# Performance work log

Hardware: AMD Instinct MI355X
Metric: run time of the kernel (lower is better)

## Reference

```python
import jax, jax.numpy as jnp
import numpy as np

MAX_LENGTH = 128
SOS_TOKEN = 0

V, H, B, S = 16384, 512, 32, 128


def gru_cell(x, h, Wih, Whh, bih, bhh):
    # torch nn.GRU gate layout: [r, z, n]
    gi = x @ Wih.T + bih  # [B, 3H]
    gh = h @ Whh.T + bhh  # [B, 3H]
    ir, iz, inn = jnp.split(gi, 3, axis=-1)
    hr, hz, hn = jnp.split(gh, 3, axis=-1)
    r = jax.nn.sigmoid(ir + hr)
    z = jax.nn.sigmoid(iz + hz)
    n = jnp.tanh(inn + r * hn)
    return (1.0 - z) * n + z * h


def setup_inputs() -> dict:
    key = jax.random.key(0)
    ks = jax.random.split(key, 13)
    w = lambda k, shape: (jax.random.normal(k, shape, dtype=jnp.float32) * 0.1)
    return {
        "input_tensor": jax.random.randint(ks[0], (B, S), 0, V),
        "enc_emb": w(ks[1], (V, H)),
        "enc_Wih": w(ks[2], (3 * H, H)),
        "enc_Whh": w(ks[3], (3 * H, H)),
        "enc_bih": w(ks[4], (3 * H,)),
        "enc_bhh": w(ks[5], (3 * H,)),
        "dec_emb": w(ks[6], (V, H)),
        "dec_Wih": w(ks[7], (3 * H, H)),
        "dec_Whh": w(ks[8], (3 * H, H)),
        "dec_bih": w(ks[9], (3 * H,)),
        "dec_bhh": w(ks[10], (3 * H,)),
        "out_W": w(ks[11], (V, H)),
        "out_b": w(ks[12], (V,)),
    }


def reference(input_tensor, enc_emb, enc_Wih, enc_Whh, enc_bih, enc_bhh,
              dec_emb, dec_Wih, dec_Whh, dec_bih, dec_bhh, out_W, out_b):
    batch = input_tensor.shape[0]

    # ---- encoder: embedding + GRU over source sequence ----
    xs = enc_emb[input_tensor]                 # [B, S, H]
    xs = jnp.swapaxes(xs, 0, 1)                # [S, B, H]

    def enc_step(h, x):
        h = gru_cell(x, h, enc_Wih, enc_Whh, enc_bih, enc_bhh)
        return h, h

    h0 = jnp.zeros((batch, H), dtype=xs.dtype)
    enc_hidden, enc_outputs = jax.lax.scan(enc_step, h0, xs)
    # enc_outputs: [S, B, H] (unused downstream, as in the original)

    # ---- decoder: free-run (target_tensor=None) with argmax feedback ----
    sos = jnp.full((batch,), SOS_TOKEN, dtype=jnp.int32)

    def dec_step(carry, _):
        h, tok = carry
        x = dec_emb[tok]                       # [B, H]
        h = gru_cell(x, h, dec_Wih, dec_Whh, dec_bih, dec_bhh)
        logits = h @ out_W.T + out_b           # [B, V]
        tok = jnp.argmax(logits, axis=-1).astype(jnp.int32)  # topk(1) feedback
        return (h, tok), logits

    (dec_hidden, _), logits = jax.lax.scan(dec_step, (enc_hidden, sos), None,
                                           length=MAX_LENGTH)
    logits = jnp.swapaxes(logits, 0, 1)        # [B, MAX_LENGTH, V]
    log_probs = jax.nn.log_softmax(logits, axis=-1)
    return log_probs, dec_hidden
```

## Files before the change

kernel.cpp:

```cpp
#include <hip/hip_runtime.h>

#define HDIM 512
#define BATCH 32
#define SEQ 128
#define VOCAB 16384
#define NBLK 256
#define NGRU 128
#define NTHR 256
#define SLOTP 32
#define HLDS_W 516

typedef unsigned long long u64;
typedef unsigned int u32;

static __device__ __forceinline__ u64 aload64(const u64* p) {
    return __hip_atomic_load(p, __ATOMIC_RELAXED, __HIP_MEMORY_SCOPE_AGENT);
}
static __device__ __forceinline__ void astore64(u64* p, u64 v) {
    __hip_atomic_store(p, v, __ATOMIC_RELAXED, __HIP_MEMORY_SCOPE_AGENT);
}
static __device__ __forceinline__ u32 aload32(const u32* p) {
    return __hip_atomic_load(p, __ATOMIC_RELAXED, __HIP_MEMORY_SCOPE_AGENT);
}
static __device__ __forceinline__ void astore32(u32* p, u32 v) {
    __hip_atomic_store(p, v, __ATOMIC_RELAXED, __HIP_MEMORY_SCOPE_AGENT);
}
static __device__ __forceinline__ void astore32f(float* p, float v) {
    __hip_atomic_store((u32*)p, __float_as_uint(v), __ATOMIC_RELAXED,
                       __HIP_MEMORY_SCOPE_AGENT);
}

static __device__ __forceinline__ float4 ld4(const float* p) {
    return *reinterpret_cast<const float4*>(p);
}
static __device__ __forceinline__ float dot4(float4 a, float4 b) {
    return a.x*b.x + a.y*b.y + a.z*b.z + a.w*b.w;
}
static __device__ __forceinline__ u32 ford(float f) {
    u32 b = __float_as_uint(f);
    return b ^ ((b >> 31) ? 0xFFFFFFFFu : 0x80000000u);
}
static __device__ __forceinline__ u64 shfl_xor_u64(u64 x, int m) {
    int lo = __shfl_xor((int)(u32)x, m);
    int hi = __shfl_xor((int)(u32)(x >> 32), m);
    return ((u64)(u32)hi << 32) | (u32)lo;
}

static __device__ __forceinline__ void pollN(const u32* slots, u32 target,
                                             int tid, int nslots) {
    if (tid < 64) {
        const int per = (nslots + 63) >> 6;
        int it = 0;
        for (;;) {
            bool ok = true;
            for (int k = 0; k < per; ++k) {
                int idx = tid * per + k;
                if (idx < nslots)
                    ok &= (aload32(&slots[idx * SLOTP]) >= target);
            }
            if (__ballot(ok) == ~0ull) break;
            if (it > 64)      __builtin_amdgcn_s_sleep(16);
            else if (it > 8)  __builtin_amdgcn_s_sleep(2);
            ++it;
        }
    }
    __syncthreads();
    asm volatile("" ::: "memory");
}

static __device__ __forceinline__ void stage_wide(float* hlf, const float* hsrc,
                                                  int tid, int blk) {
    const int rot = (blk & 63) * 64;
    #pragma unroll
    for (int g = 0; g < 2; ++g) {
        float4 v[8];
        int qs[8];
        #pragma unroll
        for (int k = 0; k < 8; ++k) {
            int q = ((g * 8 + k) * NTHR + tid + rot) & 4095;
            qs[k] = q;
            asm volatile("global_load_dwordx4 %0, %1, off sc1"
                         : "=v"(v[k]) : "v"(hsrc + q * 4));
        }
        asm volatile("s_waitcnt vmcnt(0)" ::: "memory");
        __builtin_amdgcn_sched_barrier(0);
        #pragma unroll
        for (int k = 0; k < 8; ++k) {
            int w = qs[k] * 4;
            *reinterpret_cast<float4*>(hlf + (w >> 9) * HLDS_W + (w & 511)) = v[k];
        }
    }
}

static __device__ __forceinline__ void stage_h(float* hlf, const float* hglob, int tid) {
    const u64* src = (const u64*)hglob;
    #pragma unroll
    for (int it = 0; it < 32; ++it) {
        int q = it * 256 + tid;
        int w = q * 2;
        u64 v = aload64(src + q);
        *reinterpret_cast<u64*>(hlf + (w >> 9) * HLDS_W + (w & 511)) = v;
    }
}

static __device__ __forceinline__ void gru_j(
    int j, int tid, const int* toks, const float* hlf, float* hout,
    const float* __restrict__ Wih, const float* __restrict__ Whh,
    const float* __restrict__ bih, const float* __restrict__ bhh,
    const float* __restrict__ emb)
{
    const int lane = tid & 63;
    const int kh   = lane >> 5;
    const int b    = lane & 31;

    const int tok = toks[b];
    const float* xrow = emb + (size_t)tok * HDIM + kh * 256;
    const float* hrow = hlf + b * HLDS_W + kh * 256;
    const float* wir = Wih + (size_t)(0*HDIM + j) * HDIM + kh * 256;
    const float* wiz = Wih + (size_t)(1*HDIM + j) * HDIM + kh * 256;
    const float* win = Wih + (size_t)(2*HDIM + j) * HDIM + kh * 256;
    const float* whr = Whh + (size_t)(0*HDIM + j) * HDIM + kh * 256;
    const float* whz = Whh + (size_t)(1*HDIM + j) * HDIM + kh * 256;
    const float* whn = Whh + (size_t)(2*HDIM + j) * HDIM + kh * 256;

    float pr = 0.f, pz = 0.f, pxn = 0.f, phn = 0.f;
    #pragma unroll 4
    for (int k4 = 0; k4 < 64; ++k4) {
        float4 x4 = ld4(xrow + k4*4);
        float4 h4 = ld4(hrow + k4*4);
        pr  += dot4(x4, ld4(wir + k4*4)) + dot4(h4, ld4(whr + k4*4));
        pz  += dot4(x4, ld4(wiz + k4*4)) + dot4(h4, ld4(whz + k4*4));
        pxn += dot4(x4, ld4(win + k4*4));
        phn += dot4(h4, ld4(whn + k4*4));
    }
    pr  += __shfl_xor(pr, 32);
    pz  += __shfl_xor(pz, 32);
    pxn += __shfl_xor(pxn, 32);
    phn += __shfl_xor(phn, 32);

    if (kh == 0) {
        float r = 1.f / (1.f + expf(-(pr + bih[j]      + bhh[j])));
        float z = 1.f / (1.f + expf(-(pz + bih[HDIM+j] + bhh[HDIM+j])));
        float n = tanhf(pxn + bih[2*HDIM+j] + r * (phn + bhh[2*HDIM+j]));
        float hprev = hlf[b * HLDS_W + j];
        astore32f(hout + b * HDIM + j, (1.f - z) * n + z * hprev);
    }
}

static __device__ __forceinline__ void argmax_finalize(
    int tid, const u64* pk, u64 (*redk)[8], int* tok_s)
{
    const int fb = tid >> 3, kc = tid & 7;
    const u64* p = pk + fb * NBLK;
    u64 best = aload64(p + kc);
    #pragma unroll 4
    for (int k = 1; k < 32; ++k) {
        u64 x = aload64(p + kc + k * 8);
        if (x > best) best = x;
    }
    redk[fb][kc] = best;
    __syncthreads();
    if (tid < BATCH) {
        u64 bb = redk[tid][0];
        #pragma unroll
        for (int c = 1; c < 8; ++c) { u64 x = redk[tid][c]; if (x > bb) bb = x; }
        tok_s[tid] = (int)(~(u32)bb);
    }
}

static __device__ __forceinline__ void softmax_row(float* p, int tid,
                                                   float* redm, float* reds) {
    float4 vals[16];
    float m = -3.4e38f;
    #pragma unroll
    for (int i = 0; i < 16; ++i) {
        vals[i] = ld4(p + (i * 256 + tid) * 4);
        m = fmaxf(m, fmaxf(fmaxf(vals[i].x, vals[i].y), fmaxf(vals[i].z, vals[i].w)));
    }
    #pragma unroll
    for (int d = 1; d < 64; d <<= 1) m = fmaxf(m, __shfl_xor(m, d));
    if ((tid & 63) == 0) redm[tid >> 6] = m;
    __syncthreads();
    m = fmaxf(fmaxf(redm[0], redm[1]), fmaxf(redm[2], redm[3]));
    float s = 0.f;
    #pragma unroll
    for (int i = 0; i < 16; ++i) {
        s += expf(vals[i].x - m) + expf(vals[i].y - m)
           + expf(vals[i].z - m) + expf(vals[i].w - m);
    }
    #pragma unroll
    for (int d = 1; d < 64; d <<= 1) s += __shfl_xor(s, d);
    if ((tid & 63) == 0) reds[tid >> 6] = s;
    __syncthreads();
    s = reds[0] + reds[1] + reds[2] + reds[3];
    const float lg = m + logf(s);
    #pragma unroll
    for (int i = 0; i < 16; ++i) {
        float4 r;
        r.x = vals[i].x - lg; r.y = vals[i].y - lg;
        r.z = vals[i].z - lg; r.w = vals[i].w - lg;
        *reinterpret_cast<float4*>(p + (i * 256 + tid) * 4) = r;
    }
    __syncthreads();
}

__global__ __launch_bounds__(NTHR, 1) void seq2seq_main(
    const int* __restrict__ input,
    const float* __restrict__ enc_emb, const float* __restrict__ enc_Wih,
    const float* __restrict__ enc_Whh, const float* __restrict__ enc_bih,
    const float* __restrict__ enc_bhh,
    const float* __restrict__ dec_emb, const float* __restrict__ dec_Wih,
    const float* __restrict__ dec_Whh, const float* __restrict__ dec_bih,
    const float* __restrict__ dec_bhh,
    const float* __restrict__ out_W, const float* __restrict__ out_b,
    float* __restrict__ out, float* hglob, u64* pk,
    u32* hslot, u32* pkslot)
{
    __shared__ __align__(16) float hl[BATCH][HLDS_W];
    __shared__ __align__(16) float part[4][64][33];
    __shared__ int tok_s[BATCH];
    __shared__ u64 redk[BATCH][8];

    const int tid = threadIdx.x;
    const int blk = blockIdx.x;
    float* hlf = &hl[0][0];

    for (int i = tid; i < BATCH * HLDS_W; i += NTHR) hlf[i] = 0.f;
    __syncthreads();

    const int w = tid >> 6;
    const int l = tid & 63;

    if (blk < NGRU) {
        for (int t = 0; t < SEQ; ++t) {
            float* hgo = hglob + ((t + 1) & 1) * (BATCH * HDIM);
            if (tid < BATCH) tok_s[tid] = input[tid * SEQ + t];
            __syncthreads();
            gru_j(blk * 4 + w, tid, tok_s, hlf, hgo,
                  enc_Wih, enc_Whh, enc_bih, enc_bhh, enc_emb);
            __syncthreads();
            if (tid == 0) astore32(&hslot[blk * SLOTP], (u32)(t + 1));
            pollN(hslot, (u32)(t + 1), tid, NGRU);
            stage_wide(hlf, hgo, tid, blk);
            __syncthreads();
        }
    }

    for (int t = 0; t < SEQ; ++t) {
        float* hgo = hglob + ((t + 1) & 1) * (BATCH * HDIM);

        if (blk < NGRU) {
            if (t == 0) {
                if (tid < BATCH) tok_s[tid] = 0;
                __syncthreads();
            } else {
                pollN(pkslot, (u32)t, tid, NBLK);
                argmax_finalize(tid, pk, redk, tok_s);
                __syncthreads();
            }
            gru_j(blk * 4 + w, tid, tok_s, hlf, hgo,
                  dec_Wih, dec_Whh, dec_bih, dec_bhh, dec_emb);
            __syncthreads();
            if (tid == 0) astore32(&hslot[blk * SLOTP], (u32)(SEQ + t + 1));
        }

        pollN(hslot, (u32)(SEQ + t + 1), tid, NGRU);
        stage_wide(hlf, hgo, tid, blk);
        __syncthreads();

        {
            const int ks = w;
            const int v  = blk * 64 + l;
            const float* wrow = out_W + (size_t)v * HDIM + ks * 128;
            const float* hq   = hlf + ks * 128;

            float acc[BATCH];
            #pragma unroll
            for (int b = 0; b < BATCH; ++b) acc[b] = 0.f;

            for (int k4 = 0; k4 < 32; ++k4) {
                float4 w4 = ld4(wrow + k4*4);
                #pragma unroll
                for (int b = 0; b < BATCH; ++b) {
                    float4 h4 = ld4(hq + b * HLDS_W + k4*4);
                    acc[b] += dot4(w4, h4);
                }
            }
            #pragma unroll
            for (int b = 0; b < BATCH; ++b) part[ks][l][b] = acc[b];
        }
        __syncthreads();

        {
            const int v = blk * 64 + l;
            const float vbias = out_b[v];
            #pragma unroll
            for (int i = 0; i < 8; ++i) {
                const int b = w * 8 + i;
                float s = ((part[0][l][b] + part[1][l][b]) + part[2][l][b])
                          + part[3][l][b] + vbias;
                __builtin_nontemporal_store(s,
                    &out[(size_t)b*(SEQ*VOCAB) + (size_t)t*VOCAB + v]);
                u64 key = ((u64)ford(s) << 32) | (u32)(~(u32)v);
                #pragma unroll
                for (int d = 1; d < 64; d <<= 1) {
                    u64 o = shfl_xor_u64(key, d);
                    if (o > key) key = o;
                }
                if (l == 0) astore64(&pk[b * NBLK + blk], key);
            }
        }
        __syncthreads();
        if (tid == 0) astore32(&pkslot[blk * SLOTP], (u32)(t + 1));
    }

    if (blk < 16) {
        const int idx = blk * 1024 + tid * 4;
        const int b = idx >> 9, j = idx & 511;
        *reinterpret_cast<float4*>(out + (size_t)BATCH * SEQ * VOCAB + idx) =
            *reinterpret_cast<const float4*>(&hl[b][j]);
    }
}

__global__ __launch_bounds__(256) void init_kernel(float* __restrict__ h0,
                                                   u32* __restrict__ hslot,
                                                   u32* __restrict__ pkslot) {
    int i = blockIdx.x * 256 + threadIdx.x;
    if (i < BATCH * HDIM) h0[i] = 0.f;
    if (i < NGRU * SLOTP) hslot[i] = 0;
    if (i < NBLK * SLOTP) pkslot[i] = 0;
}

__global__ __launch_bounds__(256) void gru_step_fb(
    const float* __restrict__ h_in, float* __restrict__ h_out,
    const float* __restrict__ Wih, const float* __restrict__ Whh,
    const float* __restrict__ bih, const float* __restrict__ bhh,
    const float* __restrict__ emb,
    const int* __restrict__ enc_tokens, int t, const u64* __restrict__ pk)
{
    __shared__ __align__(16) float hlt[BATCH][HLDS_W];
    __shared__ int tok_s[BATCH];
    __shared__ u64 redk[BATCH][8];
    const int tid = threadIdx.x;

    if (enc_tokens != nullptr) {
        if (tid < BATCH) tok_s[tid] = enc_tokens[tid * SEQ + t];
    } else if (t == 0) {
        if (tid < BATCH) tok_s[tid] = 0;
    } else {
        argmax_finalize(tid, pk, redk, tok_s);
    }
    stage_h(&hlt[0][0], h_in, tid);
    __syncthreads();
    gru_j(blockIdx.x * 4 + (tid >> 6), tid, tok_s, &hlt[0][0], h_out,
          Wih, Whh, bih, bhh, emb);
}

__global__ __launch_bounds__(256) void logits_fb(
    const float* __restrict__ h, const float* __restrict__ outW,
    const float* __restrict__ outb, float* __restrict__ out,
    int t, u64* __restrict__ pk)
{
    __shared__ __align__(16) float hlt[BATCH][HLDS_W];
    const int tid = threadIdx.x;
    stage_h(&hlt[0][0], h, tid);
    __syncthreads();

    const int vloc = tid & 63;
    const int bq   = tid >> 6;
    const int v    = blockIdx.x * 64 + vloc;
    const float* wrow = outW + (size_t)v * HDIM;
    const float* hlf = &hlt[0][0];

    float acc[4][8];
    #pragma unroll
    for (int q = 0; q < 4; ++q)
        #pragma unroll
        for (int i = 0; i < 8; ++i) acc[q][i] = 0.f;
    #pragma unroll
    for (int q = 0; q < 4; ++q)
        for (int k4 = 0; k4 < 32; ++k4) {
            float4 w4 = ld4(wrow + q*128 + k4*4);
            #pragma unroll
            for (int i = 0; i < 8; ++i)
                acc[q][i] += dot4(w4, ld4(hlf + (bq*8 + i) * HLDS_W + q*128 + k4*4));
        }
    const float vbias = outb[v];
    #pragma unroll
    for (int i = 0; i < 8; ++i) {
        const int b = bq*8 + i;
        float s = ((acc[0][i] + acc[1][i]) + acc[2][i]) + acc[3][i] + vbias;
        out[(size_t)b * (SEQ * VOCAB) + (size_t)t * VOCAB + v] = s;
        u64 key = ((u64)ford(s) << 32) | (u32)(~(u32)v);
        #pragma unroll
        for (int d = 1; d < 64; d <<= 1) {
            u64 o = shfl_xor_u64(key, d);
            if (o > key) key = o;
        }
        if (vloc == 0) astore64(pk + b * NBLK + blockIdx.x, key);
    }
}

__global__ __launch_bounds__(256) void copy_fb(const float* __restrict__ src,
                                               float* __restrict__ dst, int n) {
    int i = blockIdx.x * 256 + threadIdx.x;
    if (i < n) dst[i] = src[i];
}

__global__ __launch_bounds__(256) void softmax_kernel(float* __restrict__ out) {
    __shared__ float redm[4];
    __shared__ float reds[4];
    softmax_row(out + (size_t)blockIdx.x * VOCAB, threadIdx.x, redm, reds);
}

extern "C" void kernel_launch(void* const* d_in, const int* in_sizes, int n_in,
                              void* d_out, int out_size, void* d_ws, size_t ws_size,
                              hipStream_t stream) {
    const int*   input    = (const int*)  d_in[0];
    const float* enc_emb  = (const float*)d_in[1];
    const float* enc_Wih  = (const float*)d_in[2];
    const float* enc_Whh  = (const float*)d_in[3];
    const float* enc_bih  = (const float*)d_in[4];
    const float* enc_bhh  = (const float*)d_in[5];
    const float* dec_emb  = (const float*)d_in[6];
    const float* dec_Wih  = (const float*)d_in[7];
    const float* dec_Whh  = (const float*)d_in[8];
    const float* dec_bih  = (const float*)d_in[9];
    const float* dec_bhh  = (const float*)d_in[10];
    const float* out_W    = (const float*)d_in[11];
    const float* out_b    = (const float*)d_in[12];

    float* out = (float*)d_out;
    char*  ws  = (char*)d_ws;

    float* hglob  = (float*)ws;
    u64*   pk     = (u64*)(ws + 131072);
    u32*   hslot  = (u32*)(ws + 196608);
    u32*   pkslot = (u32*)(ws + 212992);

    init_kernel<<<dim3(64), dim3(256), 0, stream>>>(hglob, hslot, pkslot);

    void* args[] = {
        (void*)&input, (void*)&enc_emb, (void*)&enc_Wih, (void*)&enc_Whh,
        (void*)&enc_bih, (void*)&enc_bhh,
        (void*)&dec_emb, (void*)&dec_Wih, (void*)&dec_Whh, (void*)&dec_bih,
        (void*)&dec_bhh, (void*)&out_W, (void*)&out_b,
        (void*)&out, (void*)&hglob, (void*)&pk,
        (void*)&hslot, (void*)&pkslot
    };
    hipError_t rc = hipLaunchCooperativeKernel((void*)seq2seq_main,
                                               dim3(NBLK), dim3(NTHR),
                                               args, 0, stream);
    if (rc != hipSuccess) {
        float* hb[2] = { hglob, hglob + BATCH * HDIM };
        for (int t = 0; t < SEQ; ++t) {
            gru_step_fb<<<dim3(128), dim3(256), 0, stream>>>(
                hb[t & 1], hb[(t + 1) & 1],
                enc_Wih, enc_Whh, enc_bih, enc_bhh, enc_emb, input, t, nullptr);
        }
        for (int t = 0; t < SEQ; ++t) {
            gru_step_fb<<<dim3(128), dim3(256), 0, stream>>>(
                hb[t & 1], hb[(t + 1) & 1],
                dec_Wih, dec_Whh, dec_bih, dec_bhh, dec_emb, nullptr, t, pk);
            logits_fb<<<dim3(NBLK), dim3(256), 0, stream>>>(
                hb[(t + 1) & 1], out_W, out_b, out, t, pk);
        }
        copy_fb<<<dim3((BATCH * HDIM + 255) / 256), dim3(256), 0, stream>>>(
            hglob, out + (size_t)BATCH * SEQ * VOCAB, BATCH * HDIM);
    }

    softmax_kernel<<<dim3(BATCH * SEQ), dim3(256), 0, stream>>>(out);
}
```

Measured before the change: 11.33 ms.

## Repartition output projection by batch quarter, drop LDS reduction, prefetch weights

```diff
diff --git a/kernel.cpp b/kernel.cpp
--- a/kernel.cpp
+++ b/kernel.cpp
@@ -68,17 +68,13 @@
     asm volatile("" ::: "memory");
 }
 
-static __device__ __forceinline__ void stage_wide(float* hlf, const float* hsrc,
-                                                  int tid, int blk) {
-    const int rot = (blk & 63) * 64;
+static __device__ __forceinline__ void stage_wide(float* hlf, const float* hsrc, int tid) {
     #pragma unroll
     for (int g = 0; g < 2; ++g) {
         float4 v[8];
-        int qs[8];
         #pragma unroll
         for (int k = 0; k < 8; ++k) {
-            int q = ((g * 8 + k) * NTHR + tid + rot) & 4095;
-            qs[k] = q;
+            int q = (g * 8 + k) * NTHR + tid;
             asm volatile("global_load_dwordx4 %0, %1, off sc1"
                          : "=v"(v[k]) : "v"(hsrc + q * 4));
         }
@@ -86,7 +82,8 @@
         __builtin_amdgcn_sched_barrier(0);
         #pragma unroll
         for (int k = 0; k < 8; ++k) {
-            int w = qs[k] * 4;
+            int q = (g * 8 + k) * NTHR + tid;
+            int w = q * 4;
             *reinterpret_cast<float4*>(hlf + (w >> 9) * HLDS_W + (w & 511)) = v[k];
         }
     }
@@ -217,7 +214,6 @@
     u32* hslot, u32* pkslot)
 {
     __shared__ __align__(16) float hl[BATCH][HLDS_W];
-    __shared__ __align__(16) float part[4][64][33];
     __shared__ int tok_s[BATCH];
     __shared__ u64 redk[BATCH][8];
 
@@ -229,7 +225,9 @@
     __syncthreads();
 
     const int w = tid >> 6;
-    const int l = tid & 63;
+    const int vloc = tid & 63;
+    const int v    = blk * 64 + vloc;
+    const float* wrow = out_W + (size_t)v * HDIM;
 
     if (blk < NGRU) {
         for (int t = 0; t < SEQ; ++t) {
@@ -241,7 +239,7 @@
             __syncthreads();
             if (tid == 0) astore32(&hslot[blk * SLOTP], (u32)(t + 1));
             pollN(hslot, (u32)(t + 1), tid, NGRU);
-            stage_wide(hlf, hgo, tid, blk);
+            stage_wide(hlf, hgo, tid);
             __syncthreads();
         }
     }
@@ -264,41 +262,48 @@
             if (tid == 0) astore32(&hslot[blk * SLOTP], (u32)(SEQ + t + 1));
         }
 
+        float4 pf[8];
+        #pragma unroll
+        for (int k4 = 0; k4 < 8; ++k4) pf[k4] = ld4(wrow + k4*4);
+
         pollN(hslot, (u32)(SEQ + t + 1), tid, NGRU);
-        stage_wide(hlf, hgo, tid, blk);
+        stage_wide(hlf, hgo, tid);
         __syncthreads();
 
         {
-            const int ks = w;
-            const int v  = blk * 64 + l;
-            const float* wrow = out_W + (size_t)v * HDIM + ks * 128;
-            const float* hq   = hlf + ks * 128;
-
-            float acc[BATCH];
+            const int bq = w;
+
+            float acc[4][8];
             #pragma unroll
-            for (int b = 0; b < BATCH; ++b) acc[b] = 0.f;
+            for (int q = 0; q < 4; ++q)
+                #pragma unroll
+                for (int i = 0; i < 8; ++i) acc[q][i] = 0.f;
 
             for (int k4 = 0; k4 < 32; ++k4) {
-                float4 w4 = ld4(wrow + k4*4);
+                float4 w4 = (k4 < 8) ? pf[k4] : ld4(wrow + k4*4);
                 #pragma unroll
-                for (int b = 0; b < BATCH; ++b) {
-                    float4 h4 = ld4(hq + b * HLDS_W + k4*4);
-                    acc[b] += dot4(w4, h4);
+                for (int i = 0; i < 8; ++i) {
+                    float4 h4 = ld4(hlf + (bq*8 + i) * HLDS_W + k4*4);
+                    acc[0][i] += dot4(w4, h4);
                 }
             }
             #pragma unroll
-            for (int b = 0; b < BATCH; ++b) part[ks][l][b] = acc[b];
-        }
-        __syncthreads();
-
-        {
-            const int v = blk * 64 + l;
+            for (int q = 1; q < 4; ++q) {
+                for (int k4 = 0; k4 < 32; ++k4) {
+                    float4 w4 = ld4(wrow + q*128 + k4*4);
+                    #pragma unroll
+                    for (int i = 0; i < 8; ++i) {
+                        float4 h4 = ld4(hlf + (bq*8 + i) * HLDS_W + q*128 + k4*4);
+                        acc[q][i] += dot4(w4, h4);
+                    }
+                }
+            }
+
             const float vbias = out_b[v];
             #pragma unroll
             for (int i = 0; i < 8; ++i) {
-                const int b = w * 8 + i;
-                float s = ((part[0][l][b] + part[1][l][b]) + part[2][l][b])
-                          + part[3][l][b] + vbias;
+                const int b = bq*8 + i;
+                float s = ((acc[0][i] + acc[1][i]) + acc[2][i]) + acc[3][i] + vbias;
                 __builtin_nontemporal_store(s,
                     &out[(size_t)b*(SEQ*VOCAB) + (size_t)t*VOCAB + v]);
                 u64 key = ((u64)ford(s) << 32) | (u32)(~(u32)v);
@@ -307,7 +312,7 @@
                     u64 o = shfl_xor_u64(key, d);
                     if (o > key) key = o;
                 }
-                if (l == 0) astore64(&pk[b * NBLK + blk], key);
+                if (vloc == 0) astore64(&pk[b * NBLK + blk], key);
             }
         }
         __syncthreads();
```

Measured after the change: 25.47 ms. 2.25x slower.
